# Optimization experiments

Measured on AMD Instinct MI355X. Metric: run time of the kernel, lower is better.

Reference implementation:

```python
import jax, jax.numpy as jnp
import numpy as np

BN_EPS = 1e-5
K2 = 9  # 3x3 kernel


def _conv3x3(x, w, b):
    # x: [B,C,H,W], w: [O,C,3,3] -> [B,O,H,W], stride 1, pad 1
    out = jax.lax.conv_general_dilated(
        x, w, window_strides=(1, 1), padding=((1, 1), (1, 1)),
        dimension_numbers=("NCHW", "OIHW", "NCHW"))
    return out + b[None, :, None, None]


def setup_inputs() -> dict:
    key = jax.random.key(0)
    ks = jax.random.split(key, 8)
    B, C, H, W = 8, 256, 64, 64
    O = 256
    x = jax.random.normal(ks[0], (B, C, H, W), dtype=jnp.float32)
    # offset/mask conv: small init so sampled offsets stay near the base grid
    w_off = jax.random.normal(ks[1], (3 * K2, C, 3, 3), dtype=jnp.float32) * 0.01
    b_off = jnp.zeros((3 * K2,), dtype=jnp.float32)
    weight = jax.random.normal(ks[2], (O, C, 3, 3), dtype=jnp.float32) * 0.02
    bias = jnp.zeros((O,), dtype=jnp.float32)
    gamma = jnp.ones((O,), dtype=jnp.float32)
    beta = jnp.zeros((O,), dtype=jnp.float32)
    run_mean = jax.random.normal(ks[3], (O,), dtype=jnp.float32) * 0.1
    run_var = jax.random.uniform(ks[4], (O,), dtype=jnp.float32) + 0.5
    return {"x": x, "w_off": w_off, "b_off": b_off, "weight": weight,
            "bias": bias, "gamma": gamma, "beta": beta,
            "run_mean": run_mean, "run_var": run_var}


def _deform_sample(img, py, px):
    # img: [C,H,W]; py, px: [K2,H,W] sampling coordinates.
    # Bilinear sample with zero padding outside (DCNv2 semantics:
    # out-of-bounds corners contribute zero).
    C, H, W = img.shape
    y0 = jnp.floor(py)
    x0 = jnp.floor(px)
    wy1 = py - y0  # frac weights for the 'high' corner
    wx1 = px - x0

    def gather(yi, xi):
        valid = (yi >= 0) & (yi < H) & (xi >= 0) & (xi < W)
        yc = jnp.clip(yi, 0, H - 1).astype(jnp.int32)
        xc = jnp.clip(xi, 0, W - 1).astype(jnp.int32)
        return img[:, yc, xc] * valid.astype(img.dtype)[None]  # [C,K2,H,W]

    v00 = gather(y0, x0)
    v01 = gather(y0, x0 + 1)
    v10 = gather(y0 + 1, x0)
    v11 = gather(y0 + 1, x0 + 1)
    return (v00 * ((1 - wy1) * (1 - wx1))[None]
            + v01 * ((1 - wy1) * wx1)[None]
            + v10 * (wy1 * (1 - wx1))[None]
            + v11 * (wy1 * wx1)[None])  # [C,K2,H,W]


def reference(x, w_off, b_off, weight, bias, gamma, beta, run_mean, run_var):
    B, C, H, W = x.shape
    O = weight.shape[0]
    # 1) offset / mask branch (standard 3x3 conv)
    om = _conv3x3(x, w_off, b_off)  # [B, 27, H, W]
    off_y = om[:, :K2]
    off_x = om[:, K2:2 * K2]
    mask = jax.nn.sigmoid(om[:, 2 * K2:])  # modulation, [B,9,H,W]
    # 2) base sampling grid for 3x3, stride 1, pad 1, dilation 1
    ky = jnp.repeat(jnp.arange(3), 3).astype(x.dtype)  # [9]
    kx = jnp.tile(jnp.arange(3), 3).astype(x.dtype)    # [9]
    hs = jnp.arange(H, dtype=x.dtype)
    ws = jnp.arange(W, dtype=x.dtype)
    base_y = hs[None, :, None] - 1.0 + ky[:, None, None]  # [9,H,1]
    base_x = ws[None, None, :] - 1.0 + kx[:, None, None]  # [9,1,W]
    py = base_y[None] + off_y  # [B,9,H,W]
    px = base_x[None] + off_x
    # 3) modulated deformable im2col (bilinear gather) per batch
    cols = jax.vmap(_deform_sample)(x, py, px)  # [B,C,9,H,W]
    cols = cols * mask[:, None]                 # apply modulation mask
    # 4) GEMM over (C, K2) + bias
    w3 = weight.reshape(O, C, K2)
    out = jnp.einsum("ock,bckhw->bohw", w3, cols) + bias[None, :, None, None]
    # 5) BatchNorm (eval mode, running stats) + ReLU
    inv = gamma / jnp.sqrt(run_var + BN_EPS)
    out = out * inv[None, :, None, None] + (beta - run_mean * inv)[None, :, None, None]
    return jax.nn.relu(out)
```

## Files before the change

### kernel.cpp

```cpp
#include <hip/hip_runtime.h>
#include <math.h>

#define H 64
#define W 64
#define C 256
#define O 256
#define CK 2304
#define NB 8
#define HWSZ 4096

typedef __attribute__((ext_vector_type(8))) short short8;
typedef __attribute__((ext_vector_type(4))) float floatx4;
typedef __attribute__((ext_vector_type(4))) unsigned uintx4;

#define FSWZ(n) ((((n) & 3) << 1) | (((n) >> 2) & 1))

__device__ __forceinline__ float lo2f(unsigned u) {
  return __builtin_bit_cast(float, u << 16);
}
__device__ __forceinline__ float hi2f(unsigned u) {
  return __builtin_bit_cast(float, u & 0xffff0000u);
}
__device__ __forceinline__ unsigned pk2bf(float v0, float v1) {
  unsigned a = __builtin_bit_cast(unsigned, v0);
  unsigned b = __builtin_bit_cast(unsigned, v1);
  return ((a + 0x8000u) >> 16) | ((b + 0x8000u) & 0xffff0000u);
}

__global__ __launch_bounds__(512) void prep_x(
    const float* __restrict__ x, unsigned short* __restrict__ xt) {
  __shared__ unsigned tile[16384];
  int bid = blockIdx.x;
  int tid = threadIdx.x;
  int b = bid >> 5;
  int yg = bid & 31;
  int y0 = yg * 2;

#pragma unroll
  for (int j = 0; j < 4; ++j) {
    int e = tid + 512 * j;
    int xx4 = e & 15;
    int cp = e >> 4;
    const float* p0 = x + ((size_t)b * C + 2 * cp) * HWSZ + y0 * W + xx4 * 4;
    floatx4 f00 = *reinterpret_cast<const floatx4*>(p0);
    floatx4 f01 = *reinterpret_cast<const floatx4*>(p0 + W);
    floatx4 f10 = *reinterpret_cast<const floatx4*>(p0 + HWSZ);
    floatx4 f11 = *reinterpret_cast<const floatx4*>(p0 + HWSZ + W);
    int sw = cp & 31;
#pragma unroll
    for (int k = 0; k < 4; ++k) {
      int px = xx4 * 4 + k;
      tile[cp * 64 + (px ^ sw)] = pk2bf(f00[k], f10[k]);
      tile[8192 + cp * 64 + (px ^ sw)] = pk2bf(f01[k], f11[k]);
    }
  }
  __syncthreads();

  unsigned short* xo = xt + ((size_t)(b * 64 + y0) << 14);
#pragma unroll
  for (int j = 0; j < 8; ++j) {
    int e = tid + 512 * j;
    int cq = e & 31;
    int xx = (e >> 5) & 63;
    int r = e >> 11;
    unsigned u[4];
#pragma unroll
    for (int kk = 0; kk < 4; ++kk) {
      int cpv = cq * 4 + kk;
      u[kk] = tile[r * 8192 + cpv * 64 + (xx ^ (cpv & 31))];
    }
    uint4 v = {u[0], u[1], u[2], u[3]};
    *reinterpret_cast<uint4*>(xo + (r << 14) + (xx << 8) + (cq << 3)) = v;
  }
}

__global__ __launch_bounds__(512) void prep_wb(
    const float* __restrict__ weight, const float* __restrict__ w_off,
    const float* __restrict__ bias, const float* __restrict__ gamma,
    const float* __restrict__ beta, const float* __restrict__ run_mean,
    const float* __restrict__ run_var, unsigned short* __restrict__ wb,
    unsigned short* __restrict__ wob, float* __restrict__ invsh) {
  int bid = blockIdx.x;
  int tid = threadIdx.x;

  if (bid < 144) {
    int idx = bid * 512 + tid;
    int d0 = idx * 8;
    int lane = idx & 63;
    int mt = (idx >> 6) & 15;
    int ks = idx >> 10;
    int o = mt * 16 + (lane & 15);
    int kn0 = ks * 32 + (lane >> 4) * 8;
    int tap = kn0 >> 8;
    int c0 = kn0 & 255;
    const float* wsrc = weight + o * CK + c0 * 9 + tap;
    unsigned pk[4];
#pragma unroll
    for (int p = 0; p < 4; ++p)
      pk[p] = pk2bf(wsrc[(2 * p) * 9], wsrc[(2 * p + 1) * 9]);
    uint4 v = {pk[0], pk[1], pk[2], pk[3]};
    *reinterpret_cast<uint4*>(wb + d0) = v;
  } else if (bid < 162) {
    int idx = (bid - 144) * 512 + tid;
    int d0 = idx * 8;
    int lane = idx & 63;
    int mt = (idx >> 6) & 1;
    int ks = idx >> 7;
    int o = mt * 16 + (lane & 15);
    int kn0 = ks * 32 + (lane >> 4) * 8;
    int tap = kn0 >> 8;
    int c0 = kn0 & 255;
    uint4 v;
    if (o < 27) {
      const float* wsrc = w_off + o * CK + c0 * 9 + tap;
      unsigned pk[4];
#pragma unroll
      for (int p = 0; p < 4; ++p)
        pk[p] = pk2bf(wsrc[(2 * p) * 9], wsrc[(2 * p + 1) * 9]);
      v = (uint4){pk[0], pk[1], pk[2], pk[3]};
    } else {
      v = (uint4){0, 0, 0, 0};
    }
    *reinterpret_cast<uint4*>(wob + d0) = v;
  } else {
    if (tid < 256) {
      int o = tid;
      float inv = gamma[o] * rsqrtf(run_var[o] + 1e-5f);
      invsh[o] = inv;
      invsh[O + o] = beta[o] + (bias[o] - run_mean[o]) * inv;
    }
  }
}

__global__ __launch_bounds__(512, 4) void deform_mfma_kernel(
    const unsigned short* __restrict__ xt, const unsigned short* __restrict__ wob,
    const float* __restrict__ b_off, const unsigned short* __restrict__ wb,
    const float* __restrict__ invsh, float* __restrict__ out) {
  __shared__ short cols[64 * 256];
  __shared__ float sm_om[27 * 64];
  __shared__ int sbase[576];
  __shared__ float s00[576], s01[576], s10[576], s11[576];

  int tid = threadIdx.x;
  int lane = tid & 63;
  int wvid = tid >> 6;
  int q = lane >> 4;
  int lm = lane & 15;
  int b = blockIdx.x;
  int h = blockIdx.y;
  const unsigned short* xtb = xt + ((size_t)b << 20);

  if (wvid < 4) {
    int mt = wvid & 1;
    int nh = wvid >> 1;
    floatx4 a0[2];
    a0[0] = (floatx4){0.f, 0.f, 0.f, 0.f};
    a0[1] = (floatx4){0.f, 0.f, 0.f, 0.f};
    int pxu[2];
    pxu[0] = (nh * 2 + 0) * 16 + lm;
    pxu[1] = (nh * 2 + 1) * 16 + lm;
    for (int tap = 0; tap < 9; ++tap) {
      int yy = h - 1 + tap / 3;
      bool vy = (yy >= 0) && (yy < H);
      const unsigned short* bp[2];
      bool vv[2];
#pragma unroll
      for (int u = 0; u < 2; ++u) {
        int xx = pxu[u] - 1 + tap % 3;
        vv[u] = vy && (xx >= 0) && (xx < W);
        bp[u] = xtb + ((((yy & 63) << 6) + (xx & 63)) << 8) + q * 8;
      }
#pragma unroll
      for (int s = 0; s < 8; ++s) {
        int ks = tap * 8 + s;
        short8 afrag = *reinterpret_cast<const short8*>(
            wob + (((ks * 2 + mt) * 64 + lane) << 3));
#pragma unroll
        for (int u = 0; u < 2; ++u) {
          short8 bfrag;
          if (vv[u])
            bfrag = *reinterpret_cast<const short8*>(bp[u] + s * 32);
          else
            bfrag = (short8){0, 0, 0, 0, 0, 0, 0, 0};
          a0[u] = __builtin_amdgcn_mfma_f32_16x16x32_bf16(afrag, bfrag, a0[u], 0, 0, 0);
        }
      }
    }
#pragma unroll
    for (int u = 0; u < 2; ++u)
#pragma unroll
      for (int r = 0; r < 4; ++r) {
        int o = mt * 16 + q * 4 + r;
        if (o < 27) sm_om[o * 64 + pxu[u]] = a0[u][r] + b_off[o];
      }
  }
  __syncthreads();

  for (int e = tid; e < 576; e += 512) {
    int n = e & 63;
    int k = e >> 6;
    float oy = sm_om[k * 64 + n];
    float ox = sm_om[(9 + k) * 64 + n];
    float mv = sm_om[(18 + k) * 64 + n];
    float m = 1.0f / (1.0f + __expf(-mv));
    float py = (float)(h - 1 + k / 3) + oy;
    float px = (float)(n - 1 + k % 3) + ox;
    float yf = floorf(py), xf = floorf(px);
    int y0 = (int)yf, x0 = (int)xf;
    float fy = py - yf, fx = px - xf;
    float r0, r1; int yl;
    if (y0 >= 0 && y0 <= H - 2)      { yl = y0;    r0 = 1.f - fy; r1 = fy;       }
    else if (y0 == -1)               { yl = 0;     r0 = fy;       r1 = 0.f;      }
    else if (y0 == H - 1)            { yl = H - 2; r0 = 0.f;      r1 = 1.f - fy; }
    else                             { yl = 0;     r0 = 0.f;      r1 = 0.f;      }
    float c0, c1; int xl;
    if (x0 >= 0 && x0 <= W - 2)      { xl = x0;    c0 = 1.f - fx; c1 = fx;       }
    else if (x0 == -1)               { xl = 0;     c0 = fx;       c1 = 0.f;      }
    else if (x0 == W - 1)            { xl = W - 2; c0 = 0.f;      c1 = 1.f - fx; }
    else                             { xl = 0;     c0 = 0.f;      c1 = 0.f;      }
    r0 *= m; r1 *= m;
    sbase[e] = ((yl << 6) + xl) << 8;
    s00[e] = r0 * c0; s01[e] = r0 * c1;
    s10[e] = r1 * c0; s11[e] = r1 * c1;
  }
  __syncthreads();

  floatx4 acc[2][4];
#pragma unroll
  for (int a = 0; a < 2; ++a)
#pragma unroll
    for (int u = 0; u < 4; ++u) acc[a][u] = (floatx4){0.f, 0.f, 0.f, 0.f};

  int sn = tid >> 3;
  int scb = tid & 7;

  for (int tap = 0; tap < 9; ++tap) {
    if (tap) __syncthreads();
    {
      int ei = tap * 64 + sn;
      int base = sbase[ei];
      float w00 = s00[ei], w01 = s01[ei], w10 = s10[ei], w11 = s11[ei];
      const unsigned short* p = xtb + base;
#pragma unroll
      for (int i = 0; i < 4; ++i) {
        int cbw = (i << 3) | scb;
        int co = cbw << 3;
        uintx4 u00 = *reinterpret_cast<const uintx4*>(p + co);
        uintx4 u01 = *reinterpret_cast<const uintx4*>(p + 256 + co);
        uintx4 u10 = *reinterpret_cast<const uintx4*>(p + 16384 + co);
        uintx4 u11 = *reinterpret_cast<const uintx4*>(p + 16640 + co);
        uintx4 res;
#pragma unroll
        for (int jd = 0; jd < 4; ++jd) {
          float v0 = fmaf(w00, lo2f(u00[jd]),
                     fmaf(w01, lo2f(u01[jd]),
                     fmaf(w10, lo2f(u10[jd]), w11 * lo2f(u11[jd]))));
          float v1 = fmaf(w00, hi2f(u00[jd]),
                     fmaf(w01, hi2f(u01[jd]),
                     fmaf(w10, hi2f(u10[jd]), w11 * hi2f(u11[jd]))));
          res[jd] = pk2bf(v0, v1);
        }
        int pos = (cbw ^ FSWZ(sn)) & 31;
        *reinterpret_cast<uintx4*>(&cols[(sn << 8) + (pos << 3)]) = res;
      }
    }
    __syncthreads();

#pragma unroll
    for (int s = 0; s < 8; ++s) {
      int ks = tap * 8 + s;
      short8 afrag[2];
#pragma unroll
      for (int a = 0; a < 2; ++a)
        afrag[a] = *reinterpret_cast<const short8*>(
            wb + (((ks * 16 + wvid * 2 + a) * 64 + lane) << 3));
      short8 bfrag[4];
#pragma unroll
      for (int u = 0; u < 4; ++u) {
        int nn = u * 16 + lm;
        int pos = ((s * 4 + q) ^ FSWZ(nn)) & 31;
        bfrag[u] = *reinterpret_cast<const short8*>(&cols[(nn << 8) + (pos << 3)]);
      }
#pragma unroll
      for (int a = 0; a < 2; ++a)
#pragma unroll
        for (int u = 0; u < 4; ++u)
          acc[a][u] = __builtin_amdgcn_mfma_f32_16x16x32_bf16(
              afrag[a], bfrag[u], acc[a][u], 0, 0, 0);
    }
  }

#pragma unroll
  for (int a = 0; a < 2; ++a) {
#pragma unroll
    for (int u = 0; u < 4; ++u) {
      int nn = u * 16 + lm;
#pragma unroll
      for (int r = 0; r < 4; ++r) {
        int o = (wvid * 2 + a) * 16 + q * 4 + r;
        float v = fmaf(acc[a][u][r], invsh[o], invsh[O + o]);
        out[((size_t)(b * O + o)) * HWSZ + h * W + nn] = fmaxf(v, 0.0f);
      }
    }
  }
}

extern "C" void kernel_launch(void* const* d_in, const int* in_sizes, int n_in,
                              void* d_out, int out_size, void* d_ws, size_t ws_size,
                              hipStream_t stream) {
  const float* x        = (const float*)d_in[0];
  const float* w_off    = (const float*)d_in[1];
  const float* b_off    = (const float*)d_in[2];
  const float* weight   = (const float*)d_in[3];
  const float* bias     = (const float*)d_in[4];
  const float* gamma    = (const float*)d_in[5];
  const float* beta     = (const float*)d_in[6];
  const float* run_mean = (const float*)d_in[7];
  const float* run_var  = (const float*)d_in[8];
  float* out = (float*)d_out;

  char* ws = (char*)d_ws;
  unsigned short* xt = (unsigned short*)ws;
  unsigned short* wbf = (unsigned short*)(ws + 16777216);
  unsigned short* wob = (unsigned short*)(ws + 17956864);
  float* invsh = (float*)(ws + 18104320);

  prep_x<<<256, 512, 0, stream>>>(x, xt);
  prep_wb<<<163, 512, 0, stream>>>(weight, w_off, bias, gamma, beta,
                                   run_mean, run_var, wbf, wob, invsh);
  {
    dim3 grid(NB, H);
    deform_mfma_kernel<<<grid, 512, 0, stream>>>(xt, wob, b_off, wbf, invsh, out);
  }
}
```

Measured before the change: 192.5 us.

## Merge prep kernels, spread offset conv over all waves, packed-FMA bilinear gather

The two preprocessing kernels are merged into one launch that dispatches on block index, which removes one kernel launch. The offset/mask MFMA GEMM is now split across all 8 waves, each handling one 16-pixel tile, instead of 4 waves handling two tiles each. The bilinear interpolation uses 2-wide vector FMAs so the compiler can emit packed fp32 math. The per-tap sampling parameters are prefetched from shared memory for the next tap while the current tap's MFMA runs. The extra register pressure and changed code generation could affect occupancy.

New measurement: 193.9 us. Within noise of the previous version (+0.7%).

```diff
diff --git a/kernel.cpp b/kernel.cpp
--- a/kernel.cpp
+++ b/kernel.cpp
@@ -12,6 +12,7 @@
 typedef __attribute__((ext_vector_type(8))) short short8;
 typedef __attribute__((ext_vector_type(4))) float floatx4;
 typedef __attribute__((ext_vector_type(4))) unsigned uintx4;
+typedef __attribute__((ext_vector_type(2))) float f32x2;
 
 #define FSWZ(n) ((((n) & 3) << 1) | (((n) >> 2) & 1))
 
@@ -20,6 +21,9 @@
 }
 __device__ __forceinline__ float hi2f(unsigned u) {
   return __builtin_bit_cast(float, u & 0xffff0000u);
+}
+__device__ __forceinline__ f32x2 up2(unsigned u) {
+  return (f32x2){lo2f(u), hi2f(u)};
 }
 __device__ __forceinline__ unsigned pk2bf(float v0, float v1) {
   unsigned a = __builtin_bit_cast(unsigned, v0);
@@ -27,64 +31,58 @@
   return ((a + 0x8000u) >> 16) | ((b + 0x8000u) & 0xffff0000u);
 }
 
-__global__ __launch_bounds__(512) void prep_x(
-    const float* __restrict__ x, unsigned short* __restrict__ xt) {
+__global__ __launch_bounds__(512) void prep_all2(
+    const float* __restrict__ x, const float* __restrict__ weight,
+    const float* __restrict__ w_off, const float* __restrict__ bias,
+    const float* __restrict__ gamma, const float* __restrict__ beta,
+    const float* __restrict__ run_mean, const float* __restrict__ run_var,
+    unsigned short* __restrict__ xt, unsigned short* __restrict__ wb,
+    unsigned short* __restrict__ wob, float* __restrict__ invsh) {
   __shared__ unsigned tile[16384];
   int bid = blockIdx.x;
   int tid = threadIdx.x;
-  int b = bid >> 5;
-  int yg = bid & 31;
-  int y0 = yg * 2;
-
-#pragma unroll
-  for (int j = 0; j < 4; ++j) {
-    int e = tid + 512 * j;
-    int xx4 = e & 15;
-    int cp = e >> 4;
-    const float* p0 = x + ((size_t)b * C + 2 * cp) * HWSZ + y0 * W + xx4 * 4;
-    floatx4 f00 = *reinterpret_cast<const floatx4*>(p0);
-    floatx4 f01 = *reinterpret_cast<const floatx4*>(p0 + W);
-    floatx4 f10 = *reinterpret_cast<const floatx4*>(p0 + HWSZ);
-    floatx4 f11 = *reinterpret_cast<const floatx4*>(p0 + HWSZ + W);
-    int sw = cp & 31;
-#pragma unroll
-    for (int k = 0; k < 4; ++k) {
-      int px = xx4 * 4 + k;
-      tile[cp * 64 + (px ^ sw)] = pk2bf(f00[k], f10[k]);
-      tile[8192 + cp * 64 + (px ^ sw)] = pk2bf(f01[k], f11[k]);
-    }
-  }
-  __syncthreads();
-
-  unsigned short* xo = xt + ((size_t)(b * 64 + y0) << 14);
-#pragma unroll
-  for (int j = 0; j < 8; ++j) {
-    int e = tid + 512 * j;
-    int cq = e & 31;
-    int xx = (e >> 5) & 63;
-    int r = e >> 11;
-    unsigned u[4];
-#pragma unroll
-    for (int kk = 0; kk < 4; ++kk) {
-      int cpv = cq * 4 + kk;
-      u[kk] = tile[r * 8192 + cpv * 64 + (xx ^ (cpv & 31))];
-    }
-    uint4 v = {u[0], u[1], u[2], u[3]};
-    *reinterpret_cast<uint4*>(xo + (r << 14) + (xx << 8) + (cq << 3)) = v;
-  }
-}
-
-__global__ __launch_bounds__(512) void prep_wb(
-    const float* __restrict__ weight, const float* __restrict__ w_off,
-    const float* __restrict__ bias, const float* __restrict__ gamma,
-    const float* __restrict__ beta, const float* __restrict__ run_mean,
-    const float* __restrict__ run_var, unsigned short* __restrict__ wb,
-    unsigned short* __restrict__ wob, float* __restrict__ invsh) {
-  int bid = blockIdx.x;
-  int tid = threadIdx.x;
-
-  if (bid < 144) {
-    int idx = bid * 512 + tid;
+
+  if (bid < 256) {
+    int b = bid >> 5;
+    int yg = bid & 31;
+    int y0 = yg * 2;
+#pragma unroll
+    for (int j = 0; j < 4; ++j) {
+      int e = tid + 512 * j;
+      int xx4 = e & 15;
+      int cp = e >> 4;
+      const float* p0 = x + ((size_t)b * C + 2 * cp) * HWSZ + y0 * W + xx4 * 4;
+      floatx4 f00 = *reinterpret_cast<const floatx4*>(p0);
+      floatx4 f01 = *reinterpret_cast<const floatx4*>(p0 + W);
+      floatx4 f10 = *reinterpret_cast<const floatx4*>(p0 + HWSZ);
+      floatx4 f11 = *reinterpret_cast<const floatx4*>(p0 + HWSZ + W);
+      int sw = cp & 31;
+#pragma unroll
+      for (int k = 0; k < 4; ++k) {
+        int px = xx4 * 4 + k;
+        tile[cp * 64 + (px ^ sw)] = pk2bf(f00[k], f10[k]);
+        tile[8192 + cp * 64 + (px ^ sw)] = pk2bf(f01[k], f11[k]);
+      }
+    }
+    __syncthreads();
+    unsigned short* xo = xt + ((size_t)(b * 64 + y0) << 14);
+#pragma unroll
+    for (int j = 0; j < 8; ++j) {
+      int e = tid + 512 * j;
+      int cq = e & 31;
+      int xx = (e >> 5) & 63;
+      int r = e >> 11;
+      unsigned u[4];
+#pragma unroll
+      for (int kk = 0; kk < 4; ++kk) {
+        int cpv = cq * 4 + kk;
+        u[kk] = tile[r * 8192 + cpv * 64 + (xx ^ (cpv & 31))];
+      }
+      uint4 v = {u[0], u[1], u[2], u[3]};
+      *reinterpret_cast<uint4*>(xo + (r << 14) + (xx << 8) + (cq << 3)) = v;
+    }
+  } else if (bid < 400) {
+    int idx = (bid - 256) * 512 + tid;
     int d0 = idx * 8;
     int lane = idx & 63;
     int mt = (idx >> 6) & 15;
@@ -100,8 +98,8 @@
       pk[p] = pk2bf(wsrc[(2 * p) * 9], wsrc[(2 * p + 1) * 9]);
     uint4 v = {pk[0], pk[1], pk[2], pk[3]};
     *reinterpret_cast<uint4*>(wb + d0) = v;
-  } else if (bid < 162) {
-    int idx = (bid - 144) * 512 + tid;
+  } else if (bid < 418) {
+    int idx = (bid - 400) * 512 + tid;
     int d0 = idx * 8;
     int lane = idx & 63;
     int mt = (idx >> 6) & 1;
@@ -150,49 +148,35 @@
   int h = blockIdx.y;
   const unsigned short* xtb = xt + ((size_t)b << 20);
 
-  if (wvid < 4) {
+  {
     int mt = wvid & 1;
-    int nh = wvid >> 1;
-    floatx4 a0[2];
-    a0[0] = (floatx4){0.f, 0.f, 0.f, 0.f};
-    a0[1] = (floatx4){0.f, 0.f, 0.f, 0.f};
-    int pxu[2];
-    pxu[0] = (nh * 2 + 0) * 16 + lm;
-    pxu[1] = (nh * 2 + 1) * 16 + lm;
+    int nq = wvid >> 1;
+    floatx4 a0 = (floatx4){0.f, 0.f, 0.f, 0.f};
+    int pxn = nq * 16 + lm;
     for (int tap = 0; tap < 9; ++tap) {
       int yy = h - 1 + tap / 3;
-      bool vy = (yy >= 0) && (yy < H);
-      const unsigned short* bp[2];
-      bool vv[2];
-#pragma unroll
-      for (int u = 0; u < 2; ++u) {
-        int xx = pxu[u] - 1 + tap % 3;
-        vv[u] = vy && (xx >= 0) && (xx < W);
-        bp[u] = xtb + ((((yy & 63) << 6) + (xx & 63)) << 8) + q * 8;
-      }
+      int xx = pxn - 1 + tap % 3;
+      bool vv = (yy >= 0) && (yy < H) && (xx >= 0) && (xx < W);
+      const unsigned short* bp =
+          xtb + ((((yy & 63) << 6) + (xx & 63)) << 8) + q * 8;
 #pragma unroll
       for (int s = 0; s < 8; ++s) {
         int ks = tap * 8 + s;
         short8 afrag = *reinterpret_cast<const short8*>(
             wob + (((ks * 2 + mt) * 64 + lane) << 3));
-#pragma unroll
-        for (int u = 0; u < 2; ++u) {
-          short8 bfrag;
-          if (vv[u])
-            bfrag = *reinterpret_cast<const short8*>(bp[u] + s * 32);
-          else
-            bfrag = (short8){0, 0, 0, 0, 0, 0, 0, 0};
-          a0[u] = __builtin_amdgcn_mfma_f32_16x16x32_bf16(afrag, bfrag, a0[u], 0, 0, 0);
-        }
-      }
-    }
-#pragma unroll
-    for (int u = 0; u < 2; ++u)
-#pragma unroll
-      for (int r = 0; r < 4; ++r) {
-        int o = mt * 16 + q * 4 + r;
-        if (o < 27) sm_om[o * 64 + pxu[u]] = a0[u][r] + b_off[o];
-      }
+        short8 bfrag;
+        if (vv)
+          bfrag = *reinterpret_cast<const short8*>(bp + s * 32);
+        else
+          bfrag = (short8){0, 0, 0, 0, 0, 0, 0, 0};
+        a0 = __builtin_amdgcn_mfma_f32_16x16x32_bf16(afrag, bfrag, a0, 0, 0, 0);
+      }
+    }
+#pragma unroll
+    for (int r = 0; r < 4; ++r) {
+      int o = mt * 16 + q * 4 + r;
+      if (o < 27) sm_om[o * 64 + pxn] = a0[r] + b_off[o];
+    }
   }
   __syncthreads();
 
@@ -234,13 +218,17 @@
   int sn = tid >> 3;
   int scb = tid & 7;
 
+  int sb = sbase[sn];
+  float w00v = s00[sn], w01v = s01[sn], w10v = s10[sn], w11v = s11[sn];
+
   for (int tap = 0; tap < 9; ++tap) {
     if (tap) __syncthreads();
     {
-      int ei = tap * 64 + sn;
-      int base = sbase[ei];
-      float w00 = s00[ei], w01 = s01[ei], w10 = s10[ei], w11 = s11[ei];
-      const unsigned short* p = xtb + base;
+      const unsigned short* p = xtb + sb;
+      f32x2 W00 = (f32x2){w00v, w00v};
+      f32x2 W01 = (f32x2){w01v, w01v};
+      f32x2 W10 = (f32x2){w10v, w10v};
+      f32x2 W11 = (f32x2){w11v, w11v};
 #pragma unroll
       for (int i = 0; i < 4; ++i) {
         int cbw = (i << 3) | scb;
@@ -252,19 +240,23 @@
         uintx4 res;
 #pragma unroll
         for (int jd = 0; jd < 4; ++jd) {
-          float v0 = fmaf(w00, lo2f(u00[jd]),
-                     fmaf(w01, lo2f(u01[jd]),
-                     fmaf(w10, lo2f(u10[jd]), w11 * lo2f(u11[jd]))));
-          float v1 = fmaf(w00, hi2f(u00[jd]),
-                     fmaf(w01, hi2f(u01[jd]),
-                     fmaf(w10, hi2f(u10[jd]), w11 * hi2f(u11[jd]))));
-          res[jd] = pk2bf(v0, v1);
+          f32x2 a = up2(u00[jd]) * W00;
+          a = __builtin_elementwise_fma(up2(u01[jd]), W01, a);
+          a = __builtin_elementwise_fma(up2(u10[jd]), W10, a);
+          a = __builtin_elementwise_fma(up2(u11[jd]), W11, a);
+          res[jd] = pk2bf(a[0], a[1]);
         }
         int pos = (cbw ^ FSWZ(sn)) & 31;
         *reinterpret_cast<uintx4*>(&cols[(sn << 8) + (pos << 3)]) = res;
       }
     }
     __syncthreads();
+
+    if (tap < 8) {
+      int e2 = (tap + 1) * 64 + sn;
+      sb = sbase[e2];
+      w00v = s00[e2]; w01v = s01[e2]; w10v = s10[e2]; w11v = s11[e2];
+    }
 
 #pragma unroll
     for (int s = 0; s < 8; ++s) {
@@ -325,9 +317,8 @@
   unsigned short* wob = (unsigned short*)(ws + 17956864);
   float* invsh = (float*)(ws + 18104320);
 
-  prep_x<<<256, 512, 0, stream>>>(x, xt);
-  prep_wb<<<163, 512, 0, stream>>>(weight, w_off, bias, gamma, beta,
-                                   run_mean, run_var, wbf, wob, invsh);
+  prep_all2<<<419, 512, 0, stream>>>(x, weight, w_off, bias, gamma, beta,
+                                     run_mean, run_var, xt, wbf, wob, invsh);
   {
     dim3 grid(NB, H);
     deform_mfma_kernel<<<grid, 512, 0, stream>>>(xt, wob, b_off, wbf, invsh, out);
```
